# Kernel optimization log

Hardware: AMD Instinct MI355X
Metric: run time of the kernel (lower is better)

Reference implementation:

```python
import jax, jax.numpy as jnp
import numpy as np

B, T, C = 2, 2048, 2048
N_HEAD = 16
HS = C // N_HEAD
D_LATENT = C // 2


def setup_inputs() -> dict:
    key = jax.random.key(0)
    ks = jax.random.split(key, 7)
    s = 0.02
    return {
        "x": jax.random.normal(ks[0], (B, T, C), dtype=jnp.float32),
        "Wq": jax.random.normal(ks[1], (C, C), dtype=jnp.float32) * s,
        "Wc": jax.random.normal(ks[2], (C, D_LATENT), dtype=jnp.float32) * s,
        "Wk": jax.random.normal(ks[3], (D_LATENT, C), dtype=jnp.float32) * s,
        "Wv": jax.random.normal(ks[4], (D_LATENT, C), dtype=jnp.float32) * s,
        "Wo": jax.random.normal(ks[5], (C, C), dtype=jnp.float32) * s,
        "bo": jnp.zeros((C,), dtype=jnp.float32),
    }


def reference(x, Wq, Wc, Wk, Wv, Wo, bo):
    b, t, c = x.shape
    # projections (torch Linear without bias, weights stored as (in, out))
    q = x @ Wq                    # (B,T,C)
    c_latent = x @ Wc             # (B,T,d_latent)
    k = c_latent @ Wk             # (B,T,C)
    v = c_latent @ Wv             # (B,T,C)
    # split heads -> (B,H,T,hs)
    q = q.reshape(b, t, N_HEAD, HS).transpose(0, 2, 1, 3)
    k = k.reshape(b, t, N_HEAD, HS).transpose(0, 2, 1, 3)
    v = v.reshape(b, t, N_HEAD, HS).transpose(0, 2, 1, 3)
    scale = 1.0 / jnp.sqrt(jnp.asarray(HS, dtype=x.dtype))
    scores = jnp.einsum('bhqd,bhkd->bhqk', q, k) * scale
    causal = jnp.tril(jnp.ones((t, t), dtype=bool))
    scores = jnp.where(causal, scores, jnp.finfo(scores.dtype).min)
    attn = jax.nn.softmax(scores, axis=-1)
    y = jnp.einsum('bhqk,bhkd->bhqd', attn, v)      # (B,H,T,hs)
    y = y.transpose(0, 2, 1, 3).reshape(b, t, c)
    return y @ Wo + bo
```

## Files before the change

kernel.cpp:

```cpp
#include <hip/hip_runtime.h>
#include <hip/hip_bf16.h>
#include <math.h>

typedef __hip_bfloat16 bf16;
typedef __attribute__((ext_vector_type(8))) short bf16x8;
typedef __attribute__((ext_vector_type(4))) float f32x4;

#define B_  2
#define T_  2048
#define C_  2048
#define H_  16
#define HS_ 128
#define DL_ 1024
#define M_  (B_ * T_)
#define NQT_ (T_ / 128)

__device__ inline void lds16(const bf16* g, bf16* l) {
    __builtin_amdgcn_global_load_lds(
        (const __attribute__((address_space(1))) void*)g,
        (__attribute__((address_space(3))) void*)l, 16, 0, 0);
}

__global__ __launch_bounds__(256) void cast_bf16_k(
    const float* __restrict__ in, bf16* __restrict__ out)
{
    const size_t i = ((size_t)blockIdx.x * 256 + threadIdx.x) * 8;
    const float4 a = *(const float4*)(in + i);
    const float4 b = *(const float4*)(in + i + 4);
    bf16 o[8];
    o[0] = __float2bfloat16(a.x); o[1] = __float2bfloat16(a.y);
    o[2] = __float2bfloat16(a.z); o[3] = __float2bfloat16(a.w);
    o[4] = __float2bfloat16(b.x); o[5] = __float2bfloat16(b.y);
    o[6] = __float2bfloat16(b.z); o[7] = __float2bfloat16(b.w);
    *(uint4*)(out + i) = *(const uint4*)o;
}

__global__ __launch_bounds__(256) void transpose_cast5(
    const float* __restrict__ s0, const float* __restrict__ s1,
    const float* __restrict__ s2, const float* __restrict__ s3,
    const float* __restrict__ s4,
    bf16* __restrict__ d0, bf16* __restrict__ d1, bf16* __restrict__ d2,
    bf16* __restrict__ d3, bf16* __restrict__ d4)
{
    const float* in; bf16* out; int R, Cc;
    switch (blockIdx.z) {
        case 0: in = s0; out = d0; R = C_;  Cc = C_;  break;
        case 1: in = s1; out = d1; R = C_;  Cc = DL_; break;
        case 2: in = s2; out = d2; R = DL_; Cc = C_;  break;
        case 3: in = s3; out = d3; R = DL_; Cc = C_;  break;
        default: in = s4; out = d4; R = C_; Cc = C_;  break;
    }
    const int bx = blockIdx.x * 32, by = blockIdx.y * 32;
    if (bx >= Cc || by >= R) return;
    __shared__ float t[32][33];
    const int tx = threadIdx.x & 31, ty = threadIdx.x >> 5;
#pragma unroll
    for (int i = 0; i < 32; i += 8)
        t[ty + i][tx] = in[(size_t)(by + ty + i) * Cc + bx + tx];
    __syncthreads();
#pragma unroll
    for (int i = 0; i < 32; i += 8)
        out[(size_t)(bx + ty + i) * R + by + tx] = __float2bfloat16(t[tx][ty + i]);
}

__global__ __launch_bounds__(256) void gemm_bt_mfma(
    const bf16* __restrict__ A, const bf16* __restrict__ Bt,
    bf16* __restrict__ Cbf, float* __restrict__ Cf32,
    const float* __restrict__ bias, int M, int N, int K)
{
    __shared__ __align__(16) bf16 As[128 * 64];
    __shared__ __align__(16) bf16 Bs[128 * 64];
    const int tid  = threadIdx.x;
    const int lane = tid & 63;
    const int wave = tid >> 6;
    const int wm = wave >> 1, wn = wave & 1;
    const int quad = lane >> 4, l16 = lane & 15;
    const int sw8 = (l16 >> 1) & 7;
    const int m0 = blockIdx.y * 128, n0 = blockIdx.x * 128;

    f32x4 acc[4][4];
#pragma unroll
    for (int i = 0; i < 4; i++)
#pragma unroll
        for (int j = 0; j < 4; j++) acc[i][j] = (f32x4){0.f, 0.f, 0.f, 0.f};

    const int srow = tid >> 3;
    const int ssl  = (((tid & 7) ^ ((srow >> 1) & 7)) * 8);
    const bf16* Ap = A  + (size_t)(m0 + srow) * K + ssl;
    const bf16* Bp = Bt + (size_t)(n0 + srow) * K + ssl;
    const size_t rstr = (size_t)32 * K;

    for (int k0 = 0; k0 < K; k0 += 64) {
        if (k0) __syncthreads();
#pragma unroll
        for (int ii = 0; ii < 4; ii++) {
            lds16(Ap + ii * rstr + k0, As + ii * 2048 + tid * 8);
            lds16(Bp + ii * rstr + k0, Bs + ii * 2048 + tid * 8);
        }
        __syncthreads();

#pragma unroll
        for (int w = 0; w < 2; w++) {
            bf16x8 af[4], bfr[4];
#pragma unroll
            for (int mi = 0; mi < 4; mi++)
                af[mi] = *(const bf16x8*)&As[(wm * 64 + mi * 16 + l16) * 64 +
                                            (((w << 2) | quad) ^ sw8) * 8];
#pragma unroll
            for (int ni = 0; ni < 4; ni++)
                bfr[ni] = *(const bf16x8*)&Bs[(wn * 64 + ni * 16 + l16) * 64 +
                                              (((w << 2) | quad) ^ sw8) * 8];
#pragma unroll
            for (int mi = 0; mi < 4; mi++)
#pragma unroll
                for (int ni = 0; ni < 4; ni++)
                    acc[mi][ni] = __builtin_amdgcn_mfma_f32_16x16x32_bf16(
                        af[mi], bfr[ni], acc[mi][ni], 0, 0, 0);
        }
    }

#pragma unroll
    for (int mi = 0; mi < 4; mi++) {
#pragma unroll
        for (int ni = 0; ni < 4; ni++) {
            const int col = n0 + wn * 64 + ni * 16 + l16;
#pragma unroll
            for (int r = 0; r < 4; r++) {
                const int row = m0 + wm * 64 + mi * 16 + quad * 4 + r;
                if (Cf32)
                    Cf32[(size_t)row * N + col] = acc[mi][ni][r] + bias[col];
                else
                    Cbf[(size_t)row * N + col] = __float2bfloat16(acc[mi][ni][r]);
            }
        }
    }
}

__global__ __launch_bounds__(256) void gemm_qc_fused(
    const bf16* __restrict__ A, const bf16* __restrict__ Bt,
    bf16* __restrict__ Cq, bf16* __restrict__ Cc, int M, int K)
{
    __shared__ __align__(16) bf16 As[128 * 64];
    __shared__ __align__(16) bf16 Bs[128 * 64];
    const int tid  = threadIdx.x;
    const int lane = tid & 63;
    const int wave = tid >> 6;
    const int wm = wave >> 1, wn = wave & 1;
    const int quad = lane >> 4, l16 = lane & 15;
    const int sw8 = (l16 >> 1) & 7;
    const int m0 = blockIdx.y * 128, n0 = blockIdx.x * 128;

    f32x4 acc[4][4];
#pragma unroll
    for (int i = 0; i < 4; i++)
#pragma unroll
        for (int j = 0; j < 4; j++) acc[i][j] = (f32x4){0.f, 0.f, 0.f, 0.f};

    const int srow = tid >> 3;
    const int ssl  = (((tid & 7) ^ ((srow >> 1) & 7)) * 8);
    const bf16* Ap = A  + (size_t)(m0 + srow) * K + ssl;
    const bf16* Bp = Bt + (size_t)(n0 + srow) * K + ssl;
    const size_t rstr = (size_t)32 * K;

    for (int k0 = 0; k0 < K; k0 += 64) {
        if (k0) __syncthreads();
#pragma unroll
        for (int ii = 0; ii < 4; ii++) {
            lds16(Ap + ii * rstr + k0, As + ii * 2048 + tid * 8);
            lds16(Bp + ii * rstr + k0, Bs + ii * 2048 + tid * 8);
        }
        __syncthreads();

#pragma unroll
        for (int w = 0; w < 2; w++) {
            bf16x8 af[4], bfr[4];
#pragma unroll
            for (int mi = 0; mi < 4; mi++)
                af[mi] = *(const bf16x8*)&As[(wm * 64 + mi * 16 + l16) * 64 +
                                            (((w << 2) | quad) ^ sw8) * 8];
#pragma unroll
            for (int ni = 0; ni < 4; ni++)
                bfr[ni] = *(const bf16x8*)&Bs[(wn * 64 + ni * 16 + l16) * 64 +
                                              (((w << 2) | quad) ^ sw8) * 8];
#pragma unroll
            for (int mi = 0; mi < 4; mi++)
#pragma unroll
                for (int ni = 0; ni < 4; ni++)
                    acc[mi][ni] = __builtin_amdgcn_mfma_f32_16x16x32_bf16(
                        af[mi], bfr[ni], acc[mi][ni], 0, 0, 0);
        }
    }

    const bool is_q = (n0 < C_);
    const float scl = is_q ? 0.08838834764831845f : 1.0f;
    bf16* dst = is_q ? Cq : Cc;
    const int ld   = is_q ? C_ : DL_;
    const int coff = is_q ? 0 : C_;
#pragma unroll
    for (int mi = 0; mi < 4; mi++) {
#pragma unroll
        for (int ni = 0; ni < 4; ni++) {
            const int col = n0 - coff + wn * 64 + ni * 16 + l16;
#pragma unroll
            for (int r = 0; r < 4; r++) {
                const int row = m0 + wm * 64 + mi * 16 + quad * 4 + r;
                dst[(size_t)row * ld + col] = __float2bfloat16(acc[mi][ni][r] * scl);
            }
        }
    }
}

__global__ __launch_bounds__(512) void flash_paired(
    const bf16* __restrict__ Q, const bf16* __restrict__ K,
    const bf16* __restrict__ Vt, bf16* __restrict__ Y)
{
    __shared__ __align__(16) bf16 Ks[4][64][32];
    __shared__ __align__(16) bf16 Vs[2][128][32];
    __shared__ __align__(16) bf16 Ps[8][32][72];
    const int tid  = threadIdx.x;
    const int lane = tid & 63, wv = tid >> 6;
    const int g = wv >> 2, w4 = wv & 3;
    const int quad = lane >> 4, l16 = lane & 15;
    const int sw = (l16 >> 1) & 3;
    const int bid = blockIdx.x;
    const int bh = (bid & 7) * 4 + ((bid >> 3) & 3);
    const int pa = bid >> 5;
    const int b = bh >> 4, h = bh & 15;
    const int qt = g ? (NQT_ - 1 - pa) : pa;
    const int q0 = qt * 128;
    const int jmax_own = 2 * qt + 2;
    const int jmax = 2 * (NQT_ - 1 - pa) + 2;

    const int t2  = tid & 255;
    const int hi  = tid >> 8;
    const int sr  = t2 >> 2;
    const int ssl = ((t2 & 3) ^ ((sr >> 1) & 3)) * 8;

    bf16x8 qf[2][4];
#pragma unroll
    for (int mi = 0; mi < 2; mi++) {
        const size_t rowQ = (size_t)(b * T_ + q0 + w4 * 32 + mi * 16 + l16) * C_ + h * HS_;
#pragma unroll
        for (int c = 0; c < 4; c++)
            qf[mi][c] = *(const bf16x8*)(Q + rowQ + c * 32 + quad * 8);
    }

    f32x4 oacc[2][8];
#pragma unroll
    for (int mi = 0; mi < 2; mi++)
#pragma unroll
        for (int dt = 0; dt < 8; dt++) oacc[mi][dt] = (f32x4){0.f, 0.f, 0.f, 0.f};
    float l_s[2][4] = {{0.f,0.f,0.f,0.f},{0.f,0.f,0.f,0.f}};

    for (int j = 0; j < jmax; j++) {
        const int kv0 = j * 64;
        if (j) __syncthreads();
#pragma unroll
        for (int kc = 0; kc < 2; kc++)
            lds16(K + (size_t)(b * T_ + kv0 + sr) * C_ + h * HS_ + (hi + 2 * kc) * 32 + ssl,
                  &Ks[hi + 2 * kc][0][0] + t2 * 8);
#pragma unroll
        for (int hf = 0; hf < 2; hf++)
            lds16(Vt + (size_t)(h * HS_ + hf * 64 + sr) * M_ + b * T_ + kv0 + hi * 32 + ssl,
                  &Vs[hi][hf * 64][0] + t2 * 8);
        __syncthreads();

        if (j < jmax_own) {
            const bool act0 = (kv0 <= q0 + w4 * 32 + 15);
            const bool act1 = (kv0 <= q0 + w4 * 32 + 31);
            f32x4 sacc[2][4];
#pragma unroll
            for (int mi = 0; mi < 2; mi++)
#pragma unroll
                for (int nt = 0; nt < 4; nt++) sacc[mi][nt] = (f32x4){0.f, 0.f, 0.f, 0.f};
#pragma unroll
            for (int c = 0; c < 4; c++) {
                bf16x8 kf[4];
#pragma unroll
                for (int nt = 0; nt < 4; nt++)
                    kf[nt] = *(const bf16x8*)&Ks[c][nt * 16 + l16][(quad ^ sw) * 8];
                if (act0)
#pragma unroll
                    for (int nt = 0; nt < 4; nt++)
                        sacc[0][nt] = __builtin_amdgcn_mfma_f32_16x16x32_bf16(
                            qf[0][c], kf[nt], sacc[0][nt], 0, 0, 0);
                if (act1)
#pragma unroll
                    for (int nt = 0; nt < 4; nt++)
                        sacc[1][nt] = __builtin_amdgcn_mfma_f32_16x16x32_bf16(
                            qf[1][c], kf[nt], sacc[1][nt], 0, 0, 0);
            }
#pragma unroll
            for (int mi = 0; mi < 2; mi++) {
                const bool act = mi ? act1 : act0;
                if (!act) continue;
                const int rowbase = q0 + w4 * 32 + mi * 16;
                float p[4][4];
                if (kv0 + 63 > rowbase) {
#pragma unroll
                    for (int nt = 0; nt < 4; nt++)
#pragma unroll
                        for (int r = 0; r < 4; r++) {
                            const int col = kv0 + nt * 16 + l16;
                            const int row = rowbase + quad * 4 + r;
                            p[nt][r] = (col <= row) ? __expf(sacc[mi][nt][r]) : 0.f;
                        }
                } else {
#pragma unroll
                    for (int nt = 0; nt < 4; nt++)
#pragma unroll
                        for (int r = 0; r < 4; r++)
                            p[nt][r] = __expf(sacc[mi][nt][r]);
                }
#pragma unroll
                for (int r = 0; r < 4; r++)
                    l_s[mi][r] += p[0][r] + p[1][r] + p[2][r] + p[3][r];
#pragma unroll
                for (int nt = 0; nt < 4; nt++)
#pragma unroll
                    for (int r = 0; r < 4; r++)
                        Ps[wv][mi * 16 + quad * 4 + r][nt * 16 + l16] = __float2bfloat16(p[nt][r]);
            }
            bf16x8 pab[2][2];
#pragma unroll
            for (int mi = 0; mi < 2; mi++) {
                pab[mi][0] = *(const bf16x8*)&Ps[wv][mi * 16 + l16][quad * 8];
                pab[mi][1] = *(const bf16x8*)&Ps[wv][mi * 16 + l16][32 + quad * 8];
            }
#pragma unroll
            for (int dt = 0; dt < 8; dt++) {
                const bf16x8 vf0 = *(const bf16x8*)&Vs[0][dt * 16 + l16][(quad ^ sw) * 8];
                const bf16x8 vf1 = *(const bf16x8*)&Vs[1][dt * 16 + l16][(quad ^ sw) * 8];
                if (act0) {
                    oacc[0][dt] = __builtin_amdgcn_mfma_f32_16x16x32_bf16(pab[0][0], vf0, oacc[0][dt], 0, 0, 0);
                    oacc[0][dt] = __builtin_amdgcn_mfma_f32_16x16x32_bf16(pab[0][1], vf1, oacc[0][dt], 0, 0, 0);
                }
                if (act1) {
                    oacc[1][dt] = __builtin_amdgcn_mfma_f32_16x16x32_bf16(pab[1][0], vf0, oacc[1][dt], 0, 0, 0);
                    oacc[1][dt] = __builtin_amdgcn_mfma_f32_16x16x32_bf16(pab[1][1], vf1, oacc[1][dt], 0, 0, 0);
                }
            }
        }
    }

#pragma unroll
    for (int mi = 0; mi < 2; mi++) {
        float inv[4];
#pragma unroll
        for (int r = 0; r < 4; r++) {
            float l = l_s[mi][r];
            l += __shfl_xor(l, 1);
            l += __shfl_xor(l, 2);
            l += __shfl_xor(l, 4);
            l += __shfl_xor(l, 8);
            inv[r] = 1.f / l;
        }
        const int rowbase = q0 + w4 * 32 + mi * 16;
#pragma unroll
        for (int dt = 0; dt < 8; dt++)
#pragma unroll
            for (int r = 0; r < 4; r++)
                Y[(size_t)(b * T_ + rowbase + quad * 4 + r) * C_ + h * HS_ + dt * 16 + l16] =
                    __float2bfloat16(oacc[mi][dt][r] * inv[r]);
    }
}

extern "C" void kernel_launch(void* const* d_in, const int* in_sizes, int n_in,
                              void* d_out, int out_size, void* d_ws, size_t ws_size,
                              hipStream_t stream) {
    const float* x  = (const float*)d_in[0];
    const float* Wq = (const float*)d_in[1];
    const float* Wc = (const float*)d_in[2];
    const float* Wk = (const float*)d_in[3];
    const float* Wv = (const float*)d_in[4];
    const float* Wo = (const float*)d_in[5];
    const float* bo = (const float*)d_in[6];
    float* out = (float*)d_out;

    bf16* ws   = (bf16*)d_ws;
    bf16* x_bf = ws;
    bf16* Wq_t = x_bf + (size_t)M_ * C_;
    bf16* Wc_t = Wq_t + (size_t)C_ * C_;
    bf16* Wk_t = Wc_t + (size_t)DL_ * C_;
    bf16* Wv_t = Wk_t + (size_t)C_ * DL_;
    bf16* Wo_t = Wv_t + (size_t)C_ * DL_;
    bf16* q    = Wo_t + (size_t)C_ * C_;
    bf16* clat = q    + (size_t)M_ * C_;
    bf16* kk   = clat + (size_t)M_ * DL_;
    bf16* vt   = kk   + (size_t)M_ * C_;
    bf16* y    = vt   + (size_t)C_ * M_;

    const dim3 blk(256);

    cast_bf16_k<<<dim3((M_ * C_) / (256 * 8)), blk, 0, stream>>>(x, x_bf);
    transpose_cast5<<<dim3(C_ / 32, C_ / 32, 5), blk, 0, stream>>>(
        Wq, Wc, Wk, Wv, Wo, Wq_t, Wc_t, Wk_t, Wv_t, Wo_t);

    gemm_qc_fused<<<dim3((C_ + DL_) / 128, M_ / 128), blk, 0, stream>>>(
        x_bf, Wq_t, q, clat, M_, C_);
    gemm_bt_mfma<<<dim3(C_ / 128, M_ / 128), blk, 0, stream>>>(
        clat, Wk_t, kk, nullptr, nullptr, M_, C_, DL_);
    gemm_bt_mfma<<<dim3(M_ / 128, C_ / 128), blk, 0, stream>>>(
        Wv_t, clat, vt, nullptr, nullptr, C_, M_, DL_);

    flash_paired<<<dim3((NQT_ / 2) * H_ * B_), dim3(512), 0, stream>>>(q, kk, vt, y);

    gemm_bt_mfma<<<dim3(C_ / 128, M_ / 128), blk, 0, stream>>>(
        y, Wo_t, nullptr, out, bo, M_, C_, C_);
}
```

Baseline: 369.3 us.

## Double-buffer flash K/V tiles with dual-tile waves and fuse K/V GEMM launches

Restructures the paired-tile flash attention so every wave processes 16 rows of both the early and the late query tile. The shared K/V tile is reused across the pair, and the next K/V tile is prefetched into a second LDS buffer using vmcnt waits and raw barriers. The K and V projection GEMMs are merged into one launch of 1024 blocks, and the shared GEMM body is factored into a macro. This aims to hide global-load latency, balance causal work across waves, and cut one launch. It doubles K/V LDS usage and relies on hand-placed waitcnt counts being correct.

Measured after the change: 358.0 us. 1.03x faster.

```diff
diff --git a/kernel.cpp b/kernel.cpp
--- a/kernel.cpp
+++ b/kernel.cpp
@@ -63,62 +63,60 @@
         out[(size_t)(bx + ty + i) * R + by + tx] = __float2bfloat16(t[tx][ty + i]);
 }
 
+#define GEMM_CORE(A_, Bt_, Kdim)                                               \
+    __shared__ __align__(16) bf16 As[128 * 64];                                \
+    __shared__ __align__(16) bf16 Bs[128 * 64];                                \
+    const int tid  = threadIdx.x;                                              \
+    const int lane = tid & 63;                                                 \
+    const int wave = tid >> 6;                                                 \
+    const int wm = wave >> 1, wn = wave & 1;                                   \
+    const int quad = lane >> 4, l16 = lane & 15;                               \
+    const int sw8 = (l16 >> 1) & 7;                                            \
+    f32x4 acc[4][4];                                                           \
+    _Pragma("unroll")                                                          \
+    for (int i = 0; i < 4; i++)                                                \
+        _Pragma("unroll")                                                      \
+        for (int j = 0; j < 4; j++) acc[i][j] = (f32x4){0.f, 0.f, 0.f, 0.f};   \
+    const int srow = tid >> 3;                                                 \
+    const int ssl  = (((tid & 7) ^ ((srow >> 1) & 7)) * 8);                    \
+    const bf16* Ap = (A_)  + (size_t)(m0 + srow) * (Kdim) + ssl;               \
+    const bf16* Bp = (Bt_) + (size_t)(n0 + srow) * (Kdim) + ssl;               \
+    const size_t rstr = (size_t)32 * (Kdim);                                   \
+    for (int k0 = 0; k0 < (Kdim); k0 += 64) {                                  \
+        if (k0) __syncthreads();                                               \
+        _Pragma("unroll")                                                      \
+        for (int ii = 0; ii < 4; ii++) {                                       \
+            lds16(Ap + ii * rstr + k0, As + ii * 2048 + tid * 8);              \
+            lds16(Bp + ii * rstr + k0, Bs + ii * 2048 + tid * 8);              \
+        }                                                                      \
+        __syncthreads();                                                       \
+        _Pragma("unroll")                                                      \
+        for (int w = 0; w < 2; w++) {                                          \
+            bf16x8 af[4], bfr[4];                                              \
+            _Pragma("unroll")                                                  \
+            for (int mi = 0; mi < 4; mi++)                                     \
+                af[mi] = *(const bf16x8*)&As[(wm * 64 + mi * 16 + l16) * 64 +  \
+                                            (((w << 2) | quad) ^ sw8) * 8];    \
+            _Pragma("unroll")                                                  \
+            for (int ni = 0; ni < 4; ni++)                                     \
+                bfr[ni] = *(const bf16x8*)&Bs[(wn * 64 + ni * 16 + l16) * 64 + \
+                                              (((w << 2) | quad) ^ sw8) * 8];  \
+            _Pragma("unroll")                                                  \
+            for (int mi = 0; mi < 4; mi++)                                     \
+                _Pragma("unroll")                                              \
+                for (int ni = 0; ni < 4; ni++)                                 \
+                    acc[mi][ni] = __builtin_amdgcn_mfma_f32_16x16x32_bf16(     \
+                        af[mi], bfr[ni], acc[mi][ni], 0, 0, 0);                \
+        }                                                                      \
+    }
+
 __global__ __launch_bounds__(256) void gemm_bt_mfma(
     const bf16* __restrict__ A, const bf16* __restrict__ Bt,
     bf16* __restrict__ Cbf, float* __restrict__ Cf32,
     const float* __restrict__ bias, int M, int N, int K)
 {
-    __shared__ __align__(16) bf16 As[128 * 64];
-    __shared__ __align__(16) bf16 Bs[128 * 64];
-    const int tid  = threadIdx.x;
-    const int lane = tid & 63;
-    const int wave = tid >> 6;
-    const int wm = wave >> 1, wn = wave & 1;
-    const int quad = lane >> 4, l16 = lane & 15;
-    const int sw8 = (l16 >> 1) & 7;
     const int m0 = blockIdx.y * 128, n0 = blockIdx.x * 128;
-
-    f32x4 acc[4][4];
-#pragma unroll
-    for (int i = 0; i < 4; i++)
-#pragma unroll
-        for (int j = 0; j < 4; j++) acc[i][j] = (f32x4){0.f, 0.f, 0.f, 0.f};
-
-    const int srow = tid >> 3;
-    const int ssl  = (((tid & 7) ^ ((srow >> 1) & 7)) * 8);
-    const bf16* Ap = A  + (size_t)(m0 + srow) * K + ssl;
-    const bf16* Bp = Bt + (size_t)(n0 + srow) * K + ssl;
-    const size_t rstr = (size_t)32 * K;
-
-    for (int k0 = 0; k0 < K; k0 += 64) {
-        if (k0) __syncthreads();
-#pragma unroll
-        for (int ii = 0; ii < 4; ii++) {
-            lds16(Ap + ii * rstr + k0, As + ii * 2048 + tid * 8);
-            lds16(Bp + ii * rstr + k0, Bs + ii * 2048 + tid * 8);
-        }
-        __syncthreads();
-
-#pragma unroll
-        for (int w = 0; w < 2; w++) {
-            bf16x8 af[4], bfr[4];
-#pragma unroll
-            for (int mi = 0; mi < 4; mi++)
-                af[mi] = *(const bf16x8*)&As[(wm * 64 + mi * 16 + l16) * 64 +
-                                            (((w << 2) | quad) ^ sw8) * 8];
-#pragma unroll
-            for (int ni = 0; ni < 4; ni++)
-                bfr[ni] = *(const bf16x8*)&Bs[(wn * 64 + ni * 16 + l16) * 64 +
-                                              (((w << 2) | quad) ^ sw8) * 8];
-#pragma unroll
-            for (int mi = 0; mi < 4; mi++)
-#pragma unroll
-                for (int ni = 0; ni < 4; ni++)
-                    acc[mi][ni] = __builtin_amdgcn_mfma_f32_16x16x32_bf16(
-                        af[mi], bfr[ni], acc[mi][ni], 0, 0, 0);
-        }
-    }
-
+    GEMM_CORE(A, Bt, K)
 #pragma unroll
     for (int mi = 0; mi < 4; mi++) {
 #pragma unroll
@@ -140,57 +138,8 @@
     const bf16* __restrict__ A, const bf16* __restrict__ Bt,
     bf16* __restrict__ Cq, bf16* __restrict__ Cc, int M, int K)
 {
-    __shared__ __align__(16) bf16 As[128 * 64];
-    __shared__ __align__(16) bf16 Bs[128 * 64];
-    const int tid  = threadIdx.x;
-    const int lane = tid & 63;
-    const int wave = tid >> 6;
-    const int wm = wave >> 1, wn = wave & 1;
-    const int quad = lane >> 4, l16 = lane & 15;
-    const int sw8 = (l16 >> 1) & 7;
     const int m0 = blockIdx.y * 128, n0 = blockIdx.x * 128;
-
-    f32x4 acc[4][4];
-#pragma unroll
-    for (int i = 0; i < 4; i++)
-#pragma unroll
-        for (int j = 0; j < 4; j++) acc[i][j] = (f32x4){0.f, 0.f, 0.f, 0.f};
-
-    const int srow = tid >> 3;
-    const int ssl  = (((tid & 7) ^ ((srow >> 1) & 7)) * 8);
-    const bf16* Ap = A  + (size_t)(m0 + srow) * K + ssl;
-    const bf16* Bp = Bt + (size_t)(n0 + srow) * K + ssl;
-    const size_t rstr = (size_t)32 * K;
-
-    for (int k0 = 0; k0 < K; k0 += 64) {
-        if (k0) __syncthreads();
-#pragma unroll
-        for (int ii = 0; ii < 4; ii++) {
-            lds16(Ap + ii * rstr + k0, As + ii * 2048 + tid * 8);
-            lds16(Bp + ii * rstr + k0, Bs + ii * 2048 + tid * 8);
-        }
-        __syncthreads();
-
-#pragma unroll
-        for (int w = 0; w < 2; w++) {
-            bf16x8 af[4], bfr[4];
-#pragma unroll
-            for (int mi = 0; mi < 4; mi++)
-                af[mi] = *(const bf16x8*)&As[(wm * 64 + mi * 16 + l16) * 64 +
-                                            (((w << 2) | quad) ^ sw8) * 8];
-#pragma unroll
-            for (int ni = 0; ni < 4; ni++)
-                bfr[ni] = *(const bf16x8*)&Bs[(wn * 64 + ni * 16 + l16) * 64 +
-                                              (((w << 2) | quad) ^ sw8) * 8];
-#pragma unroll
-            for (int mi = 0; mi < 4; mi++)
-#pragma unroll
-                for (int ni = 0; ni < 4; ni++)
-                    acc[mi][ni] = __builtin_amdgcn_mfma_f32_16x16x32_bf16(
-                        af[mi], bfr[ni], acc[mi][ni], 0, 0, 0);
-        }
-    }
-
+    GEMM_CORE(A, Bt, K)
     const bool is_q = (n0 < C_);
     const float scl = is_q ? 0.08838834764831845f : 1.0f;
     bf16* dst = is_q ? Cq : Cc;
@@ -210,159 +159,176 @@
     }
 }
 
-__global__ __launch_bounds__(512) void flash_paired(
+__global__ __launch_bounds__(256) void gemm_kv_fused(
+    const bf16* __restrict__ clat, const bf16* __restrict__ Wk_t,
+    const bf16* __restrict__ Wv_t, bf16* __restrict__ kk, bf16* __restrict__ vt)
+{
+    const int bid = blockIdx.x;
+    const bf16 *A, *Bt; bf16* dst; int N, m0, n0;
+    if (bid < 512) { A = clat; Bt = Wk_t; dst = kk; N = C_;
+                     m0 = (bid >> 4) * 128; n0 = (bid & 15) * 128; }
+    else           { const int t = bid - 512;
+                     A = Wv_t; Bt = clat; dst = vt; N = M_;
+                     m0 = (t >> 5) * 128; n0 = (t & 31) * 128; }
+    GEMM_CORE(A, Bt, DL_)
+#pragma unroll
+    for (int mi = 0; mi < 4; mi++) {
+#pragma unroll
+        for (int ni = 0; ni < 4; ni++) {
+            const int col = n0 + wn * 64 + ni * 16 + l16;
+#pragma unroll
+            for (int r = 0; r < 4; r++) {
+                const int row = m0 + wm * 64 + mi * 16 + quad * 4 + r;
+                dst[(size_t)row * N + col] = __float2bfloat16(acc[mi][ni][r]);
+            }
+        }
+    }
+}
+
+__global__ __launch_bounds__(512) void flash_dual(
     const bf16* __restrict__ Q, const bf16* __restrict__ K,
     const bf16* __restrict__ Vt, bf16* __restrict__ Y)
 {
-    __shared__ __align__(16) bf16 Ks[4][64][32];
-    __shared__ __align__(16) bf16 Vs[2][128][32];
-    __shared__ __align__(16) bf16 Ps[8][32][72];
+    __shared__ __align__(16) bf16 Ks[2][4][64][32];
+    __shared__ __align__(16) bf16 Vs[2][2][128][32];
+    __shared__ __align__(16) bf16 Ps[8][16][72];
     const int tid  = threadIdx.x;
     const int lane = tid & 63, wv = tid >> 6;
-    const int g = wv >> 2, w4 = wv & 3;
     const int quad = lane >> 4, l16 = lane & 15;
     const int sw = (l16 >> 1) & 3;
     const int bid = blockIdx.x;
     const int bh = (bid & 7) * 4 + ((bid >> 3) & 3);
     const int pa = bid >> 5;
     const int b = bh >> 4, h = bh & 15;
-    const int qt = g ? (NQT_ - 1 - pa) : pa;
-    const int q0 = qt * 128;
-    const int jmax_own = 2 * qt + 2;
-    const int jmax = 2 * (NQT_ - 1 - pa) + 2;
+    const int qA0 = pa * 128, qB0 = (NQT_ - 1 - pa) * 128;
+    const int jA = 2 * pa + 2;
+    const int jB = 2 * (NQT_ - 1 - pa) + 2;
 
     const int t2  = tid & 255;
     const int hi  = tid >> 8;
     const int sr  = t2 >> 2;
     const int ssl = ((t2 & 3) ^ ((sr >> 1) & 3)) * 8;
 
-    bf16x8 qf[2][4];
-#pragma unroll
-    for (int mi = 0; mi < 2; mi++) {
-        const size_t rowQ = (size_t)(b * T_ + q0 + w4 * 32 + mi * 16 + l16) * C_ + h * HS_;
-#pragma unroll
-        for (int c = 0; c < 4; c++)
-            qf[mi][c] = *(const bf16x8*)(Q + rowQ + c * 32 + quad * 8);
-    }
-
-    f32x4 oacc[2][8];
-#pragma unroll
-    for (int mi = 0; mi < 2; mi++)
-#pragma unroll
-        for (int dt = 0; dt < 8; dt++) oacc[mi][dt] = (f32x4){0.f, 0.f, 0.f, 0.f};
-    float l_s[2][4] = {{0.f,0.f,0.f,0.f},{0.f,0.f,0.f,0.f}};
-
-    for (int j = 0; j < jmax; j++) {
+    bf16x8 qfA[4], qfB[4];
+    {
+        const size_t rA = (size_t)(b * T_ + qA0 + wv * 16 + l16) * C_ + h * HS_;
+        const size_t rB = (size_t)(b * T_ + qB0 + wv * 16 + l16) * C_ + h * HS_;
+#pragma unroll
+        for (int c = 0; c < 4; c++) {
+            qfA[c] = *(const bf16x8*)(Q + rA + c * 32 + quad * 8);
+            qfB[c] = *(const bf16x8*)(Q + rB + c * 32 + quad * 8);
+        }
+    }
+
+    f32x4 oA[8], oB[8];
+#pragma unroll
+    for (int dt = 0; dt < 8; dt++) {
+        oA[dt] = (f32x4){0.f, 0.f, 0.f, 0.f};
+        oB[dt] = (f32x4){0.f, 0.f, 0.f, 0.f};
+    }
+    float lA[4] = {0.f, 0.f, 0.f, 0.f}, lB[4] = {0.f, 0.f, 0.f, 0.f};
+
+    auto stage = [&](int j, int buf) {
         const int kv0 = j * 64;
-        if (j) __syncthreads();
 #pragma unroll
         for (int kc = 0; kc < 2; kc++)
             lds16(K + (size_t)(b * T_ + kv0 + sr) * C_ + h * HS_ + (hi + 2 * kc) * 32 + ssl,
-                  &Ks[hi + 2 * kc][0][0] + t2 * 8);
+                  &Ks[buf][hi + 2 * kc][0][0] + t2 * 8);
 #pragma unroll
         for (int hf = 0; hf < 2; hf++)
             lds16(Vt + (size_t)(h * HS_ + hf * 64 + sr) * M_ + b * T_ + kv0 + hi * 32 + ssl,
-                  &Vs[hi][hf * 64][0] + t2 * 8);
-        __syncthreads();
-
-        if (j < jmax_own) {
-            const bool act0 = (kv0 <= q0 + w4 * 32 + 15);
-            const bool act1 = (kv0 <= q0 + w4 * 32 + 31);
-            f32x4 sacc[2][4];
-#pragma unroll
-            for (int mi = 0; mi < 2; mi++)
-#pragma unroll
-                for (int nt = 0; nt < 4; nt++) sacc[mi][nt] = (f32x4){0.f, 0.f, 0.f, 0.f};
-#pragma unroll
-            for (int c = 0; c < 4; c++) {
-                bf16x8 kf[4];
-#pragma unroll
-                for (int nt = 0; nt < 4; nt++)
-                    kf[nt] = *(const bf16x8*)&Ks[c][nt * 16 + l16][(quad ^ sw) * 8];
-                if (act0)
-#pragma unroll
-                    for (int nt = 0; nt < 4; nt++)
-                        sacc[0][nt] = __builtin_amdgcn_mfma_f32_16x16x32_bf16(
-                            qf[0][c], kf[nt], sacc[0][nt], 0, 0, 0);
-                if (act1)
-#pragma unroll
-                    for (int nt = 0; nt < 4; nt++)
-                        sacc[1][nt] = __builtin_amdgcn_mfma_f32_16x16x32_bf16(
-                            qf[1][c], kf[nt], sacc[1][nt], 0, 0, 0);
-            }
-#pragma unroll
-            for (int mi = 0; mi < 2; mi++) {
-                const bool act = mi ? act1 : act0;
-                if (!act) continue;
-                const int rowbase = q0 + w4 * 32 + mi * 16;
-                float p[4][4];
-                if (kv0 + 63 > rowbase) {
-#pragma unroll
-                    for (int nt = 0; nt < 4; nt++)
-#pragma unroll
-                        for (int r = 0; r < 4; r++) {
-                            const int col = kv0 + nt * 16 + l16;
-                            const int row = rowbase + quad * 4 + r;
-                            p[nt][r] = (col <= row) ? __expf(sacc[mi][nt][r]) : 0.f;
-                        }
-                } else {
-#pragma unroll
-                    for (int nt = 0; nt < 4; nt++)
-#pragma unroll
-                        for (int r = 0; r < 4; r++)
-                            p[nt][r] = __expf(sacc[mi][nt][r]);
+                  &Vs[buf][hi][hf * 64][0] + t2 * 8);
+    };
+
+    auto tile = [&](int buf, int kv0, int q0, const bf16x8* qf, f32x4* oacc, float* l_s) {
+        const int rowbase = q0 + wv * 16;
+        if (kv0 > rowbase + 15) return;
+        f32x4 sacc[4];
+#pragma unroll
+        for (int nt = 0; nt < 4; nt++) sacc[nt] = (f32x4){0.f, 0.f, 0.f, 0.f};
+#pragma unroll
+        for (int c = 0; c < 4; c++) {
+            bf16x8 kf[4];
+#pragma unroll
+            for (int nt = 0; nt < 4; nt++)
+                kf[nt] = *(const bf16x8*)&Ks[buf][c][nt * 16 + l16][(quad ^ sw) * 8];
+#pragma unroll
+            for (int nt = 0; nt < 4; nt++)
+                sacc[nt] = __builtin_amdgcn_mfma_f32_16x16x32_bf16(qf[c], kf[nt], sacc[nt], 0, 0, 0);
+        }
+        float p[4][4];
+        if (kv0 + 63 > rowbase) {
+#pragma unroll
+            for (int nt = 0; nt < 4; nt++)
+#pragma unroll
+                for (int r = 0; r < 4; r++) {
+                    const int col = kv0 + nt * 16 + l16;
+                    const int row = rowbase + quad * 4 + r;
+                    p[nt][r] = (col <= row) ? __expf(sacc[nt][r]) : 0.f;
                 }
+        } else {
+#pragma unroll
+            for (int nt = 0; nt < 4; nt++)
 #pragma unroll
                 for (int r = 0; r < 4; r++)
-                    l_s[mi][r] += p[0][r] + p[1][r] + p[2][r] + p[3][r];
-#pragma unroll
-                for (int nt = 0; nt < 4; nt++)
-#pragma unroll
-                    for (int r = 0; r < 4; r++)
-                        Ps[wv][mi * 16 + quad * 4 + r][nt * 16 + l16] = __float2bfloat16(p[nt][r]);
-            }
-            bf16x8 pab[2][2];
-#pragma unroll
-            for (int mi = 0; mi < 2; mi++) {
-                pab[mi][0] = *(const bf16x8*)&Ps[wv][mi * 16 + l16][quad * 8];
-                pab[mi][1] = *(const bf16x8*)&Ps[wv][mi * 16 + l16][32 + quad * 8];
-            }
-#pragma unroll
-            for (int dt = 0; dt < 8; dt++) {
-                const bf16x8 vf0 = *(const bf16x8*)&Vs[0][dt * 16 + l16][(quad ^ sw) * 8];
-                const bf16x8 vf1 = *(const bf16x8*)&Vs[1][dt * 16 + l16][(quad ^ sw) * 8];
-                if (act0) {
-                    oacc[0][dt] = __builtin_amdgcn_mfma_f32_16x16x32_bf16(pab[0][0], vf0, oacc[0][dt], 0, 0, 0);
-                    oacc[0][dt] = __builtin_amdgcn_mfma_f32_16x16x32_bf16(pab[0][1], vf1, oacc[0][dt], 0, 0, 0);
-                }
-                if (act1) {
-                    oacc[1][dt] = __builtin_amdgcn_mfma_f32_16x16x32_bf16(pab[1][0], vf0, oacc[1][dt], 0, 0, 0);
-                    oacc[1][dt] = __builtin_amdgcn_mfma_f32_16x16x32_bf16(pab[1][1], vf1, oacc[1][dt], 0, 0, 0);
-                }
-            }
-        }
-    }
-
-#pragma unroll
-    for (int mi = 0; mi < 2; mi++) {
+                    p[nt][r] = __expf(sacc[nt][r]);
+        }
+#pragma unroll
+        for (int r = 0; r < 4; r++)
+            l_s[r] += p[0][r] + p[1][r] + p[2][r] + p[3][r];
+#pragma unroll
+        for (int nt = 0; nt < 4; nt++)
+#pragma unroll
+            for (int r = 0; r < 4; r++)
+                Ps[wv][quad * 4 + r][nt * 16 + l16] = __float2bfloat16(p[nt][r]);
+        const bf16x8 pa0 = *(const bf16x8*)&Ps[wv][l16][quad * 8];
+        const bf16x8 pa1 = *(const bf16x8*)&Ps[wv][l16][32 + quad * 8];
+#pragma unroll
+        for (int dt = 0; dt < 8; dt++) {
+            const bf16x8 vf0 = *(const bf16x8*)&Vs[buf][0][dt * 16 + l16][(quad ^ sw) * 8];
+            const bf16x8 vf1 = *(const bf16x8*)&Vs[buf][1][dt * 16 + l16][(quad ^ sw) * 8];
+            oacc[dt] = __builtin_amdgcn_mfma_f32_16x16x32_bf16(pa0, vf0, oacc[dt], 0, 0, 0);
+            oacc[dt] = __builtin_amdgcn_mfma_f32_16x16x32_bf16(pa1, vf1, oacc[dt], 0, 0, 0);
+        }
+    };
+
+    stage(0, 0);
+    for (int j = 0; j < jB; j++) {
+        const int kv0 = j * 64;
+        if (j + 1 < jB) {
+            stage(j + 1, (j + 1) & 1);
+            __asm__ __volatile__("s_waitcnt vmcnt(4)" ::: "memory");
+        } else {
+            __asm__ __volatile__("s_waitcnt vmcnt(0)" ::: "memory");
+        }
+        __builtin_amdgcn_s_barrier();
+        tile(j & 1, kv0, qB0, qfB, oB, lB);
+        if (j < jA) tile(j & 1, kv0, qA0, qfA, oA, lA);
+        __asm__ __volatile__("s_waitcnt lgkmcnt(0)" ::: "memory");
+        __builtin_amdgcn_s_barrier();
+    }
+
+    auto finish = [&](int q0, f32x4* oacc, float* l_s) {
         float inv[4];
 #pragma unroll
         for (int r = 0; r < 4; r++) {
-            float l = l_s[mi][r];
+            float l = l_s[r];
             l += __shfl_xor(l, 1);
             l += __shfl_xor(l, 2);
             l += __shfl_xor(l, 4);
             l += __shfl_xor(l, 8);
             inv[r] = 1.f / l;
         }
-        const int rowbase = q0 + w4 * 32 + mi * 16;
+        const int rowbase = q0 + wv * 16;
 #pragma unroll
         for (int dt = 0; dt < 8; dt++)
 #pragma unroll
             for (int r = 0; r < 4; r++)
                 Y[(size_t)(b * T_ + rowbase + quad * 4 + r) * C_ + h * HS_ + dt * 16 + l16] =
-                    __float2bfloat16(oacc[mi][dt][r] * inv[r]);
-    }
+                    __float2bfloat16(oacc[dt][r] * inv[r]);
+    };
+    finish(qA0, oA, lA);
+    finish(qB0, oB, lB);
 }
 
 extern "C" void kernel_launch(void* const* d_in, const int* in_sizes, int n_in,
@@ -398,12 +364,9 @@
 
     gemm_qc_fused<<<dim3((C_ + DL_) / 128, M_ / 128), blk, 0, stream>>>(
         x_bf, Wq_t, q, clat, M_, C_);
-    gemm_bt_mfma<<<dim3(C_ / 128, M_ / 128), blk, 0, stream>>>(
-        clat, Wk_t, kk, nullptr, nullptr, M_, C_, DL_);
-    gemm_bt_mfma<<<dim3(M_ / 128, C_ / 128), blk, 0, stream>>>(
-        Wv_t, clat, vt, nullptr, nullptr, C_, M_, DL_);
-
-    flash_paired<<<dim3((NQT_ / 2) * H_ * B_), dim3(512), 0, stream>>>(q, kk, vt, y);
+    gemm_kv_fused<<<dim3(1024), blk, 0, stream>>>(clat, Wk_t, Wv_t, kk, vt);
+
+    flash_dual<<<dim3((NQT_ / 2) * H_ * B_), dim3(512), 0, stream>>>(q, kk, vt, y);
 
     gemm_bt_mfma<<<dim3(C_ / 128, M_ / 128), blk, 0, stream>>>(
         y, Wo_t, nullptr, out, bo, M_, C_, C_);
```
